# Performance work log

Measured on AMD Instinct MI355X. Metric: run time of the kernel, lower is better.

## Reference

```python
import jax, jax.numpy as jnp
import numpy as np

N = 100000  # nodes
EPS_BN = 1e-5
EPS_NORM = 1e-12


def sage_conv(x, edge_index, wl, bl, wr):
    # PyG SAGEConv (aggr='mean', normalize=True, project=False):
    # out = lin_l(mean_{j in N(i)} x_j) + lin_r(x_i); then L2-normalize rows.
    src, dst = edge_index[0], edge_index[1]
    msgs = x[src]                                            # [E, C] gather
    agg = jax.ops.segment_sum(msgs, dst, num_segments=N)     # [N, C]
    cnt = jax.ops.segment_sum(jnp.ones((edge_index.shape[1],), x.dtype), dst,
                              num_segments=N)                # [N]
    agg = agg / jnp.maximum(cnt, 1.0)[:, None]               # mean (0 for isolated)
    out = agg @ wl.T + bl + x @ wr.T                         # lin_l has bias, lin_r doesn't
    nrm = jnp.sqrt(jnp.sum(out * out, axis=-1, keepdims=True))
    return out / jnp.maximum(nrm, EPS_NORM)


def batch_norm(x, gamma, beta):
    # BatchNorm1d in training mode: batch stats, biased variance
    mean = jnp.mean(x, axis=0)
    var = jnp.mean((x - mean) ** 2, axis=0)
    return gamma * (x - mean) * jax.lax.rsqrt(var + EPS_BN) + beta


def setup_inputs() -> dict:
    key = jax.random.key(0)
    ks = jax.random.split(key, 9)
    C_in, C_h, C_out = 128, 128, 47
    E = 800000
    x = jax.random.normal(ks[0], (N, C_in), dtype=jnp.float32)
    edge_index = jax.random.randint(ks[1], (2, E), 0, N, dtype=jnp.int64)
    s = 0.1
    return {
        "x": x,
        "edge_index": edge_index,
        "w1l": jax.random.normal(ks[2], (C_h, C_in), dtype=jnp.float32) * s,
        "b1l": jnp.zeros((C_h,), dtype=jnp.float32),
        "w1r": jax.random.normal(ks[3], (C_h, C_in), dtype=jnp.float32) * s,
        "bn_gamma": jnp.ones((C_h,), dtype=jnp.float32),
        "bn_beta": jnp.zeros((C_h,), dtype=jnp.float32),
        "w2l": jax.random.normal(ks[4], (C_out, C_h), dtype=jnp.float32) * s,
        "b2l": jnp.zeros((C_out,), dtype=jnp.float32),
        "w2r": jax.random.normal(ks[5], (C_out, C_h), dtype=jnp.float32) * s,
    }


def reference(x, edge_index, w1l, b1l, w1r, bn_gamma, bn_beta, w2l, b2l, w2r):
    h = sage_conv(x, edge_index, w1l, b1l, w1r)   # [N, 128]
    h = batch_norm(h, bn_gamma, bn_beta)
    h = jax.nn.relu(h)
    # dropout p=0.0 -> identity
    out = sage_conv(h, edge_index, w2l, b2l, w2r)  # [N, 47]
    return out
```

## Files before the change

### kernel.cpp

```cpp
#include <hip/hip_runtime.h>
#include <cstdint>


typedef __attribute__((ext_vector_type(8))) short s8v;
typedef __attribute__((ext_vector_type(4))) short s4v;
typedef __attribute__((ext_vector_type(4))) float fx4;

#define CSR_CHUNK 8192
#define CSR_SH 8
#define CSR_NBPAD 512
#define CSR_BUFCAP 3072

static __device__ __forceinline__ float bf2f(unsigned short h) {
    union { unsigned int u; float f; } c; c.u = (unsigned int)h << 16; return c.f;
}
static __device__ __forceinline__ unsigned short f2bf(float f) {
    union { float f; unsigned int u; } c; c.f = f;
    unsigned int u = c.u;
    return (unsigned short)((u + 0x7FFF + ((u >> 16) & 1)) >> 16);
}

__global__ __launch_bounds__(256) void k_prep(
        const float* __restrict__ x, const float* __restrict__ w1l,
        const float* __restrict__ w1r, const float* __restrict__ w2l,
        const float* __restrict__ w2r, const int* __restrict__ ei,
        unsigned short* __restrict__ xb, unsigned short* __restrict__ wB1,
        unsigned short* __restrict__ wB2p, float* __restrict__ stats,
        int* __restrict__ counts, int n, int nE, int prepBlocks) {
    __shared__ int hist[CSR_NBPAD];
    int t = threadIdx.x;
    if ((int)blockIdx.x >= prepBlocks) {
        int chunk = blockIdx.x - prepBlocks;
        hist[t] = 0; hist[t + 256] = 0;
        __syncthreads();
        int e0 = chunk * CSR_CHUNK;
        int e1 = min(e0 + CSR_CHUNK, nE);
        for (int e = e0 + t; e < e1; e += 256)
            atomicAdd(&hist[ei[nE + e] >> CSR_SH], 1);
        __syncthreads();
        counts[chunk * CSR_NBPAD + t] = hist[t];
        counts[chunk * CSR_NBPAD + t + 256] = hist[t + 256];
        return;
    }
    int idx = blockIdx.x * 256 + t;
    int nx = n * 16;
    if (idx < nx) {
        float4 a = ((const float4*)x)[idx * 2];
        float4 b = ((const float4*)x)[idx * 2 + 1];
        union { s8v v; unsigned short u[8]; } o;
        o.u[0] = f2bf(a.x); o.u[1] = f2bf(a.y); o.u[2] = f2bf(a.z); o.u[3] = f2bf(a.w);
        o.u[4] = f2bf(b.x); o.u[5] = f2bf(b.y); o.u[6] = f2bf(b.z); o.u[7] = f2bf(b.w);
        ((s8v*)xb)[idx] = o.v;
        return;
    }
    idx -= nx;
    if (idx < 32768) {
        int j = idx >> 8, k = idx & 255;
        float v = (k < 128) ? w1l[j * 128 + k] : w1r[j * 128 + (k - 128)];
        wB1[idx] = f2bf(v);
        return;
    }
    idx -= 32768;
    if (idx < 16384) {
        int j = idx >> 7, k = idx & 127;
        float v = 0.f;
        if (j < 47)      v = w2l[j * 128 + k];
        else if (j < 94) v = w2r[(j - 47) * 128 + k];
        wB2p[idx] = f2bf(v);
        return;
    }
    idx -= 16384;
    if (idx < 256) stats[idx] = 0.f;
}

__global__ __launch_bounds__(256) void k_bmeta(
        const int* __restrict__ counts, int* __restrict__ bucketStart,
        int* __restrict__ gcur, int nCh, int NB) {
    __shared__ int tot[CSR_NBPAD], tot2[CSR_NBPAD], sh[256], bs[CSR_NBPAD];
    int t = threadIdx.x;
    int tl = t & 127, g = t >> 7;
    int half = (nCh + 1) >> 1;
    int c0 = g * half, c1 = min(nCh, c0 + half);
    int4 s4 = {0, 0, 0, 0};
    for (int c = c0; c < c1; ++c) {
        int4 v = *(const int4*)(counts + (size_t)c * CSR_NBPAD + tl * 4);
        s4.x += v.x; s4.y += v.y; s4.z += v.z; s4.w += v.w;
    }
    *(int4*)((g ? tot2 : tot) + tl * 4) = s4;
    __syncthreads();
    tot[t] += tot2[t];
    tot[t + 256] += tot2[t + 256];
    __syncthreads();
    int pairSum = tot[2 * t] + tot[2 * t + 1];
    sh[t] = pairSum;
    __syncthreads();
    for (int off = 1; off < 256; off <<= 1) {
        int add = (t >= off) ? sh[t - off] : 0;
        __syncthreads();
        sh[t] += add;
        __syncthreads();
    }
    int excl = sh[t] - pairSum;
    bs[2 * t] = excl;
    bs[2 * t + 1] = excl + tot[2 * t];
    __syncthreads();
    for (int b = t; b <= NB; b += 256) bucketStart[b] = bs[b];
    for (int b = t; b < CSR_NBPAD; b += 256) gcur[b] = bs[b];
}

__global__ __launch_bounds__(256) void k_bfill(
        const int* __restrict__ ei, const int* __restrict__ counts,
        int* __restrict__ gcur, int* __restrict__ pairs, int nE) {
    __shared__ int cur[CSR_NBPAD];
    int t = threadIdx.x;
    #pragma unroll
    for (int i = 0; i < 2; ++i) {
        int b = t + i * 256;
        int h = counts[blockIdx.x * CSR_NBPAD + b];
        cur[b] = h ? atomicAdd(&gcur[b], h) : 0;
    }
    __syncthreads();
    int e0 = blockIdx.x * CSR_CHUNK;
    int e1 = min(e0 + CSR_CHUNK, nE);
    for (int e = e0 + t; e < e1; e += 256) {
        int s = ei[e];
        int d = ei[nE + e];
        int p = atomicAdd(&cur[d >> CSR_SH], 1);
        pairs[p] = (s << 8) | (d & 255);
    }
}

__global__ __launch_bounds__(256) void k_csr(
        const int* __restrict__ pairs, const int* __restrict__ bucketStart,
        int* __restrict__ deg, int* __restrict__ rowStart,
        int* __restrict__ srcIdx, int n) {
    __shared__ int cnt[256], scn[256], cur[256];
    __shared__ int buf[CSR_BUFCAP];
    int t = threadIdx.x;
    int bkt = blockIdx.x;
    int eBeg = bucketStart[bkt], eEnd = bucketStart[bkt + 1];
    int node0 = bkt << CSR_SH;
    cnt[t] = 0;
    __syncthreads();
    for (int e = eBeg + t; e < eEnd; e += 256)
        atomicAdd(&cnt[pairs[e] & 255], 1);
    __syncthreads();
    int myc = cnt[t];
    scn[t] = myc;
    __syncthreads();
    for (int off = 1; off < 256; off <<= 1) {
        int add = (t >= off) ? scn[t - off] : 0;
        __syncthreads();
        scn[t] += add;
        __syncthreads();
    }
    int excl = scn[t] - myc;
    cur[t] = excl;
    int node = node0 + t;
    if (node < n) { deg[node] = myc; rowStart[node] = eBeg + excl; }
    __syncthreads();
    for (int e = eBeg + t; e < eEnd; e += 256) {
        int pk = pairs[e];
        int p = atomicAdd(&cur[pk & 255], 1);
        int src = pk >> 8;
        if (p < CSR_BUFCAP) buf[p] = src;
        else srcIdx[eBeg + p] = src;
    }
    __syncthreads();
    int m = min(eEnd - eBeg, CSR_BUFCAP);
    for (int i = t; i < m; i += 256) srcIdx[eBeg + i] = buf[i];
}

__global__ __launch_bounds__(256) void k_gather1(
        const unsigned short* __restrict__ xb, const int* __restrict__ rowStart,
        const int* __restrict__ deg, const int* __restrict__ srcIdx,
        unsigned short* __restrict__ aggb, int n) {
    int t = threadIdx.x;
    int q = t & 15, grp = t >> 4;
    int node = blockIdx.x * 16 + grp;
    if (node >= n) return;
    int beg = rowStart[node];
    int d = deg[node];
    int end = beg + d;
    float a0[8] = {}, a1[8] = {}, a2[8] = {}, a3[8] = {};
    int e = beg;
    for (; e + 4 <= end; e += 4) {
        int s0 = srcIdx[e], s1v = srcIdx[e + 1], s2 = srcIdx[e + 2], s3 = srcIdx[e + 3];
        s8v v0 = *(const s8v*)(xb + (size_t)s0 * 128 + q * 8);
        s8v v1 = *(const s8v*)(xb + (size_t)s1v * 128 + q * 8);
        s8v v2 = *(const s8v*)(xb + (size_t)s2 * 128 + q * 8);
        s8v v3 = *(const s8v*)(xb + (size_t)s3 * 128 + q * 8);
        #pragma unroll
        for (int u = 0; u < 8; ++u) {
            a0[u] += bf2f((unsigned short)v0[u]);
            a1[u] += bf2f((unsigned short)v1[u]);
            a2[u] += bf2f((unsigned short)v2[u]);
            a3[u] += bf2f((unsigned short)v3[u]);
        }
    }
    for (; e < end; ++e) {
        s8v v0 = *(const s8v*)(xb + (size_t)srcIdx[e] * 128 + q * 8);
        #pragma unroll
        for (int u = 0; u < 8; ++u) a0[u] += bf2f((unsigned short)v0[u]);
    }
    float ic = 1.0f / fmaxf((float)d, 1.0f);
    union { s8v v; unsigned short u[8]; } o;
    #pragma unroll
    for (int u = 0; u < 8; ++u)
        o.u[u] = f2bf((a0[u] + a1[u] + a2[u] + a3[u]) * ic);
    *(s8v*)(aggb + (size_t)node * 128 + q * 8) = o.v;
}

__global__ __launch_bounds__(256, 3) void k_gemm1(
        const unsigned short* __restrict__ xb, const unsigned short* __restrict__ aggb,
        const unsigned short* __restrict__ wB1, const float* __restrict__ b1l,
        unsigned short* __restrict__ s1b, float* __restrict__ stats, int n) {
    __shared__ float norm2[256];
    __shared__ float invn[128];
    __shared__ float statS[256];
    __shared__ float statQ[256];
    int t = threadIdx.x;
    int w = t >> 6, L = t & 63;
    int q = L >> 4, lm = L & 15;
    int wr0 = (w >> 1) * 64;
    int wc0 = (w & 1) * 64;
    int r0 = blockIdx.x * 128;

    int arow[4], brow[4];
    #pragma unroll
    for (int r = 0; r < 4; ++r) {
        int gr = r0 + wr0 + r * 16 + lm;
        arow[r] = gr < n ? gr : (n - 1);
        brow[r] = wc0 + r * 16 + lm;
    }

    fx4 acc[4][4];
    fx4 z4 = {0.f, 0.f, 0.f, 0.f};
    #pragma unroll
    for (int r = 0; r < 4; ++r)
        #pragma unroll
        for (int c = 0; c < 4; ++c) acc[r][c] = z4;

    #pragma unroll
    for (int kt = 0; kt < 8; ++kt) {
        const unsigned short* src = (kt < 4) ? aggb : xb;
        int kb = (kt & 3) * 32 + q * 8;
        s8v af[4], bfr[4];
        #pragma unroll
        for (int r = 0; r < 4; ++r)
            af[r] = *(const s8v*)(src + (size_t)arow[r] * 128 + kb);
        #pragma unroll
        for (int c = 0; c < 4; ++c)
            bfr[c] = *(const s8v*)(wB1 + (size_t)brow[c] * 256 + kt * 32 + q * 8);
        #pragma unroll
        for (int r = 0; r < 4; ++r)
            #pragma unroll
            for (int c = 0; c < 4; ++c)
                acc[r][c] = __builtin_amdgcn_mfma_f32_16x16x32_bf16(af[r], bfr[c], acc[r][c], 0, 0, 0);
    }

    float bj[4];
    #pragma unroll
    for (int c = 0; c < 4; ++c) bj[c] = b1l[wc0 + c * 16 + lm];
    #pragma unroll
    for (int r = 0; r < 4; ++r)
        #pragma unroll
        for (int c = 0; c < 4; ++c) acc[r][c] += bj[c];

    fx4 pr[4];
    #pragma unroll
    for (int r = 0; r < 4; ++r) {
        fx4 p = acc[r][0] * acc[r][0];
        #pragma unroll
        for (int c = 1; c < 4; ++c) p += acc[r][c] * acc[r][c];
        #pragma unroll
        for (int off = 1; off <= 8; off <<= 1)
            #pragma unroll
            for (int i2 = 0; i2 < 4; ++i2) p[i2] += __shfl_xor(p[i2], off, 64);
        pr[r] = p;
    }

    if (lm == 0) {
        #pragma unroll
        for (int r = 0; r < 4; ++r)
            #pragma unroll
            for (int i = 0; i < 4; ++i)
                norm2[(wr0 + r * 16 + q * 4 + i) * 2 + (w & 1)] = pr[r][i];
    }
    __syncthreads();
    if (t < 128) {
        float s = norm2[t * 2] + norm2[t * 2 + 1];
        invn[t] = 1.0f / fmaxf(sqrtf(s), 1e-12f);
    }
    __syncthreads();

    float cS[4] = {}, cQ[4] = {};
    #pragma unroll
    for (int r = 0; r < 4; ++r) {
        int rowb = wr0 + r * 16 + q * 4;
        fx4 iv = *(const fx4*)&invn[rowb];
        #pragma unroll
        for (int c = 0; c < 4; ++c) {
            fx4 v = acc[r][c] * iv;
            int col = wc0 + c * 16 + lm;
            #pragma unroll
            for (int i = 0; i < 4; ++i) {
                int gr = r0 + rowb + i;
                if (gr < n) {
                    s1b[(size_t)gr * 128 + col] = f2bf(v[i]);
                    cS[c] += v[i];
                    cQ[c] += v[i] * v[i];
                }
            }
        }
    }
    #pragma unroll
    for (int off = 16; off <= 32; off <<= 1)
        #pragma unroll
        for (int c = 0; c < 4; ++c) {
            cS[c] += __shfl_xor(cS[c], off, 64);
            cQ[c] += __shfl_xor(cQ[c], off, 64);
        }
    if (q == 0) {
        #pragma unroll
        for (int c = 0; c < 4; ++c) {
            int col = wc0 + c * 16 + lm;
            statS[col * 2 + (w >> 1)] = cS[c];
            statQ[col * 2 + (w >> 1)] = cQ[c];
        }
    }
    __syncthreads();
    if (t < 128) {
        atomicAdd(&stats[t],       statS[t * 2] + statS[t * 2 + 1]);
        atomicAdd(&stats[128 + t], statQ[t * 2] + statQ[t * 2 + 1]);
    }
}

__global__ __launch_bounds__(256, 3) void k_gemm2(
        const unsigned short* __restrict__ s1b, const unsigned short* __restrict__ wB2p,
        const float* __restrict__ stats, const float* __restrict__ gamma,
        const float* __restrict__ beta, const float* __restrict__ b2l,
        unsigned short* __restrict__ y2b, float* __restrict__ rbuf, int n) {
    __shared__ __align__(16) float abuf[128];
    __shared__ __align__(16) float bbuf[128];
    int t = threadIdx.x;
    int w = t >> 6, L = t & 63;
    int q = L >> 4, lm = L & 15;
    int wr0 = (w >> 1) * 64, wc0 = (w & 1) * 64;
    int r0 = blockIdx.x * 128;

    if (t < 128) {
        float s = stats[t], qv = stats[128 + t];
        float fn = (float)n;
        float mean = s / fn;
        float var = qv / fn - mean * mean;
        float istd = rsqrtf(var + 1e-5f);
        float a = gamma[t] * istd;
        abuf[t] = a;
        bbuf[t] = beta[t] - mean * a;
    }
    __syncthreads();

    int arow[4], brow[4];
    #pragma unroll
    for (int r = 0; r < 4; ++r) {
        int gr = r0 + wr0 + r * 16 + lm;
        arow[r] = gr < n ? gr : (n - 1);
        brow[r] = wc0 + r * 16 + lm;
    }

    fx4 acc[4][4];
    fx4 z4 = {0.f, 0.f, 0.f, 0.f};
    #pragma unroll
    for (int r = 0; r < 4; ++r)
        #pragma unroll
        for (int c = 0; c < 4; ++c) acc[r][c] = z4;

    #pragma unroll
    for (int kt = 0; kt < 4; ++kt) {
        int kb = kt * 32 + q * 8;
        fx4 a0 = *(const fx4*)&abuf[kb];
        fx4 a1 = *(const fx4*)&abuf[kb + 4];
        fx4 b0 = *(const fx4*)&bbuf[kb];
        fx4 b1 = *(const fx4*)&bbuf[kb + 4];
        s8v af[4], bfr[4];
        #pragma unroll
        for (int r = 0; r < 4; ++r) {
            s8v sv = *(const s8v*)(s1b + (size_t)arow[r] * 128 + kb);
            union { s8v v; unsigned short u[8]; } o;
            #pragma unroll
            for (int u = 0; u < 4; ++u) {
                float h0 = fmaxf(fmaf(a0[u], bf2f((unsigned short)sv[u]), b0[u]), 0.f);
                float h1 = fmaxf(fmaf(a1[u], bf2f((unsigned short)sv[u + 4]), b1[u]), 0.f);
                o.u[u]     = f2bf(h0);
                o.u[u + 4] = f2bf(h1);
            }
            af[r] = o.v;
        }
        #pragma unroll
        for (int c = 0; c < 4; ++c)
            bfr[c] = *(const s8v*)(wB2p + (size_t)brow[c] * 128 + kb);
        #pragma unroll
        for (int r = 0; r < 4; ++r)
            #pragma unroll
            for (int c = 0; c < 4; ++c)
                acc[r][c] = __builtin_amdgcn_mfma_f32_16x16x32_bf16(af[r], bfr[c], acc[r][c], 0, 0, 0);
    }

    #pragma unroll
    for (int c = 0; c < 4; ++c) {
        int col = wc0 + c * 16 + lm;
        float bb = (col >= 47 && col < 94) ? b2l[col - 47] : 0.f;
        #pragma unroll
        for (int r = 0; r < 4; ++r) {
            int rowb = wr0 + r * 16 + q * 4;
            #pragma unroll
            for (int i = 0; i < 4; ++i) {
                int gr = r0 + rowb + i;
                if (gr >= n) continue;
                float v = acc[r][c][i];
                if (col < 47)      y2b[(size_t)gr * 64 + col] = f2bf(v);
                else if (col < 94) rbuf[(size_t)gr * 48 + (col - 47)] = v + bb;
            }
        }
    }
}

__global__ __launch_bounds__(256) void k_gather2_final(
        const unsigned short* __restrict__ y2b, const float* __restrict__ rbuf,
        const int* __restrict__ rowStart, const int* __restrict__ deg,
        const int* __restrict__ srcIdx, float* __restrict__ out, int n) {
    int t = threadIdx.x;
    int q = t & 15, grp = t >> 4;
    int node = blockIdx.x * 16 + grp;
    if (node >= n) return;
    int beg = rowStart[node];
    int d = deg[node];
    int end = beg + d;
    float acc[4] = {0.f, 0.f, 0.f, 0.f};
    int e = beg;
    for (; e + 8 <= end; e += 8) {
        int s0 = srcIdx[e],     s1v = srcIdx[e + 1];
        int s2 = srcIdx[e + 2], s3  = srcIdx[e + 3];
        int s4 = srcIdx[e + 4], s5  = srcIdx[e + 5];
        int s6 = srcIdx[e + 6], s7  = srcIdx[e + 7];
        s4v v0 = *(const s4v*)(y2b + (size_t)s0 * 64 + q * 4);
        s4v v1 = *(const s4v*)(y2b + (size_t)s1v * 64 + q * 4);
        s4v v2 = *(const s4v*)(y2b + (size_t)s2 * 64 + q * 4);
        s4v v3 = *(const s4v*)(y2b + (size_t)s3 * 64 + q * 4);
        s4v v4 = *(const s4v*)(y2b + (size_t)s4 * 64 + q * 4);
        s4v v5 = *(const s4v*)(y2b + (size_t)s5 * 64 + q * 4);
        s4v v6 = *(const s4v*)(y2b + (size_t)s6 * 64 + q * 4);
        s4v v7 = *(const s4v*)(y2b + (size_t)s7 * 64 + q * 4);
        #pragma unroll
        for (int u = 0; u < 4; ++u) {
            acc[u] += (bf2f((unsigned short)v0[u]) + bf2f((unsigned short)v1[u]))
                    + (bf2f((unsigned short)v2[u]) + bf2f((unsigned short)v3[u]))
                    + (bf2f((unsigned short)v4[u]) + bf2f((unsigned short)v5[u]))
                    + (bf2f((unsigned short)v6[u]) + bf2f((unsigned short)v7[u]));
        }
    }
    for (; e + 4 <= end; e += 4) {
        int s0 = srcIdx[e],     s1v = srcIdx[e + 1];
        int s2 = srcIdx[e + 2], s3  = srcIdx[e + 3];
        s4v v0 = *(const s4v*)(y2b + (size_t)s0 * 64 + q * 4);
        s4v v1 = *(const s4v*)(y2b + (size_t)s1v * 64 + q * 4);
        s4v v2 = *(const s4v*)(y2b + (size_t)s2 * 64 + q * 4);
        s4v v3 = *(const s4v*)(y2b + (size_t)s3 * 64 + q * 4);
        #pragma unroll
        for (int u = 0; u < 4; ++u)
            acc[u] += (bf2f((unsigned short)v0[u]) + bf2f((unsigned short)v1[u]))
                    + (bf2f((unsigned short)v2[u]) + bf2f((unsigned short)v3[u]));
    }
    for (; e < end; ++e) {
        s4v v0 = *(const s4v*)(y2b + (size_t)srcIdx[e] * 64 + q * 4);
        #pragma unroll
        for (int u = 0; u < 4; ++u) acc[u] += bf2f((unsigned short)v0[u]);
    }
    float ic = 1.0f / fmaxf((float)d, 1.0f);
    fx4 rb = *(const fx4*)(rbuf + (size_t)node * 48 + q * 4);
    float vi[4];
    float ss = 0.f;
    #pragma unroll
    for (int u = 0; u < 4; ++u) {
        int ch = q * 4 + u;
        float v = (ch < 47) ? (acc[u] * ic + rb[u]) : 0.f;
        vi[u] = v;
        ss += v * v;
    }
    #pragma unroll
    for (int off = 1; off <= 8; off <<= 1) ss += __shfl_xor(ss, off, 64);
    float inv = 1.0f / fmaxf(sqrtf(ss), 1e-12f);
    #pragma unroll
    for (int u = 0; u < 4; ++u) {
        int ch = q * 4 + u;
        if (ch < 47) out[(size_t)node * 47 + ch] = vi[u] * inv;
    }
}

extern "C" void kernel_launch(void* const* d_in, const int* in_sizes, int n_in,
                              void* d_out, int out_size, void* d_ws, size_t ws_size,
                              hipStream_t stream) {
    const float* x     = (const float*)d_in[0];
    const int*   ei    = (const int*)d_in[1];
    const float* w1l   = (const float*)d_in[2];
    const float* b1l   = (const float*)d_in[3];
    const float* w1r   = (const float*)d_in[4];
    const float* gamma = (const float*)d_in[5];
    const float* beta  = (const float*)d_in[6];
    const float* w2l   = (const float*)d_in[7];
    const float* b2l   = (const float*)d_in[8];
    const float* w2r   = (const float*)d_in[9];
    float* out = (float*)d_out;

    int n  = in_sizes[0] / 128;
    int nE = in_sizes[1] / 2;

    int NB  = (n + 255) >> 8;
    int nCh = (nE + CSR_CHUNK - 1) / CSR_CHUNK;

    int* deg       = (int*)d_ws;
    float* stats   = (float*)(deg + n);
    int* rowStart  = (int*)(stats + 256);
    int* meta      = rowStart + n;
    int* srcIdx    = meta + n;
    unsigned short* xb   = (unsigned short*)(srcIdx + nE);
    unsigned short* aggb = xb + (size_t)n * 128;
    unsigned short* s1b  = aggb + (size_t)n * 128;
    unsigned short* wB1  = s1b + (size_t)n * 128;
    unsigned short* wB2p = wB1 + 32768;
    int* counts      = meta;
    int* bucketStart = meta + 60000;
    int* gcur        = meta + 61000;
    int* pairs       = (int*)s1b;
    unsigned short* y2b = xb;
    float* rbuf = (float*)(y2b + (size_t)n * 64);

    int prepTotal  = n * 16 + 32768 + 16384 + 256;
    int prepBlocks = (prepTotal + 255) / 256;

    k_prep<<<prepBlocks + nCh, 256, 0, stream>>>(
        x, w1l, w1r, w2l, w2r, ei, xb, wB1, wB2p, stats, counts, n, nE, prepBlocks);
    k_bmeta<<<1, 256, 0, stream>>>(counts, bucketStart, gcur, nCh, NB);
    k_bfill<<<nCh, 256, 0, stream>>>(ei, counts, gcur, pairs, nE);
    k_csr<<<NB, 256, 0, stream>>>(pairs, bucketStart, deg, rowStart, srcIdx, n);
    k_gather1<<<(n + 15) / 16, 256, 0, stream>>>(xb, rowStart, deg, srcIdx, aggb, n);
    k_gemm1<<<(n + 127) / 128, 256, 0, stream>>>(xb, aggb, wB1, b1l, s1b, stats, n);
    k_gemm2<<<(n + 127) / 128, 256, 0, stream>>>(
        s1b, wB2p, stats, gamma, beta, b2l, y2b, rbuf, n);
    k_gather2_final<<<(n + 15) / 16, 256, 0, stream>>>(y2b, rbuf, rowStart, deg, srcIdx, out, n);
}
```

Measured before the change: 298.7 us.

## Stage GEMM operand tiles in LDS via async global_load_lds with XOR swizzle

Both GEMM kernels now copy their whole A tile (aggregated/input features or layer-1 activations) and the weight tile into shared memory with direct global-to-LDS 16-byte loads before computing. Previously each lane read its MFMA fragments straight from global memory. The layout uses an XOR swizzle to avoid bank conflicts, and the loads are issued up front so they can coalesce. In exchange, LDS use rises sharply (about 128 KB in gemm1), occupancy bounds drop to 1 and 2 blocks per CU, and there is no overlap between the copy and the compute.

```diff
diff --git a/kernel.cpp b/kernel.cpp
--- a/kernel.cpp
+++ b/kernel.cpp
@@ -211,10 +211,17 @@
     *(s8v*)(aggb + (size_t)node * 128 + q * 8) = o.v;
 }
 
-__global__ __launch_bounds__(256, 3) void k_gemm1(
+#define GLL16(GSRC, LDST) \
+    __builtin_amdgcn_global_load_lds( \
+        (__attribute__((address_space(1))) void*)(void*)(GSRC), \
+        (__attribute__((address_space(3))) void*)(LDST), 16, 0, 0)
+
+__global__ __launch_bounds__(256, 1) void k_gemm1(
         const unsigned short* __restrict__ xb, const unsigned short* __restrict__ aggb,
         const unsigned short* __restrict__ wB1, const float* __restrict__ b1l,
         unsigned short* __restrict__ s1b, float* __restrict__ stats, int n) {
+    __shared__ __align__(16) unsigned short xs[128 * 256];
+    __shared__ __align__(16) unsigned short ws[128 * 256];
     __shared__ float norm2[256];
     __shared__ float invn[128];
     __shared__ float statS[256];
@@ -226,13 +233,16 @@
     int wc0 = (w & 1) * 64;
     int r0 = blockIdx.x * 128;
 
-    int arow[4], brow[4];
-    #pragma unroll
-    for (int r = 0; r < 4; ++r) {
-        int gr = r0 + wr0 + r * 16 + lm;
-        arow[r] = gr < n ? gr : (n - 1);
-        brow[r] = wc0 + r * 16 + lm;
-    }
+    for (int i = t; i < 4096; i += 256) {
+        int row = i >> 5, p = i & 31;
+        int sl = p ^ (row & 7);
+        int gr = r0 + row; gr = gr < n ? gr : (n - 1);
+        const unsigned short* sp = (sl < 16) ? (aggb + (size_t)gr * 128 + sl * 8)
+                                             : (xb + (size_t)gr * 128 + (sl - 16) * 8);
+        GLL16(sp, &xs[i * 8]);
+        GLL16(wB1 + (size_t)row * 256 + sl * 8, &ws[i * 8]);
+    }
+    __syncthreads();
 
     fx4 acc[4][4];
     fx4 z4 = {0.f, 0.f, 0.f, 0.f};
@@ -243,15 +253,18 @@
 
     #pragma unroll
     for (int kt = 0; kt < 8; ++kt) {
-        const unsigned short* src = (kt < 4) ? aggb : xb;
-        int kb = (kt & 3) * 32 + q * 8;
+        int slot = kt * 4 + q;
         s8v af[4], bfr[4];
         #pragma unroll
-        for (int r = 0; r < 4; ++r)
-            af[r] = *(const s8v*)(src + (size_t)arow[r] * 128 + kb);
-        #pragma unroll
-        for (int c = 0; c < 4; ++c)
-            bfr[c] = *(const s8v*)(wB1 + (size_t)brow[c] * 256 + kt * 32 + q * 8);
+        for (int r = 0; r < 4; ++r) {
+            int row = wr0 + r * 16 + lm;
+            af[r] = *(const s8v*)&xs[row * 256 + ((slot ^ (row & 7)) << 3)];
+        }
+        #pragma unroll
+        for (int c = 0; c < 4; ++c) {
+            int row = wc0 + c * 16 + lm;
+            bfr[c] = *(const s8v*)&ws[row * 256 + ((slot ^ (row & 7)) << 3)];
+        }
         #pragma unroll
         for (int r = 0; r < 4; ++r)
             #pragma unroll
@@ -336,11 +349,13 @@
     }
 }
 
-__global__ __launch_bounds__(256, 3) void k_gemm2(
+__global__ __launch_bounds__(256, 2) void k_gemm2(
         const unsigned short* __restrict__ s1b, const unsigned short* __restrict__ wB2p,
         const float* __restrict__ stats, const float* __restrict__ gamma,
         const float* __restrict__ beta, const float* __restrict__ b2l,
         unsigned short* __restrict__ y2b, float* __restrict__ rbuf, int n) {
+    __shared__ __align__(16) unsigned short xs[128 * 128];
+    __shared__ __align__(16) unsigned short ws[128 * 128];
     __shared__ __align__(16) float abuf[128];
     __shared__ __align__(16) float bbuf[128];
     int t = threadIdx.x;
@@ -359,15 +374,15 @@
         abuf[t] = a;
         bbuf[t] = beta[t] - mean * a;
     }
-    __syncthreads();
-
-    int arow[4], brow[4];
-    #pragma unroll
-    for (int r = 0; r < 4; ++r) {
-        int gr = r0 + wr0 + r * 16 + lm;
-        arow[r] = gr < n ? gr : (n - 1);
-        brow[r] = wc0 + r * 16 + lm;
-    }
+
+    for (int i = t; i < 2048; i += 256) {
+        int row = i >> 4, p = i & 15;
+        int sl = p ^ (row & 7);
+        int gr = r0 + row; gr = gr < n ? gr : (n - 1);
+        GLL16(s1b + (size_t)gr * 128 + sl * 8, &xs[i * 8]);
+        GLL16(wB2p + (size_t)row * 128 + sl * 8, &ws[i * 8]);
+    }
+    __syncthreads();
 
     fx4 acc[4][4];
     fx4 z4 = {0.f, 0.f, 0.f, 0.f};
@@ -378,6 +393,7 @@
 
     #pragma unroll
     for (int kt = 0; kt < 4; ++kt) {
+        int slot = kt * 4 + q;
         int kb = kt * 32 + q * 8;
         fx4 a0 = *(const fx4*)&abuf[kb];
         fx4 a1 = *(const fx4*)&abuf[kb + 4];
@@ -386,7 +402,8 @@
         s8v af[4], bfr[4];
         #pragma unroll
         for (int r = 0; r < 4; ++r) {
-            s8v sv = *(const s8v*)(s1b + (size_t)arow[r] * 128 + kb);
+            int row = wr0 + r * 16 + lm;
+            s8v sv = *(const s8v*)&xs[row * 128 + ((slot ^ (row & 7)) << 3)];
             union { s8v v; unsigned short u[8]; } o;
             #pragma unroll
             for (int u = 0; u < 4; ++u) {
@@ -398,8 +415,10 @@
             af[r] = o.v;
         }
         #pragma unroll
-        for (int c = 0; c < 4; ++c)
-            bfr[c] = *(const s8v*)(wB2p + (size_t)brow[c] * 128 + kb);
+        for (int c = 0; c < 4; ++c) {
+            int row = wc0 + c * 16 + lm;
+            bfr[c] = *(const s8v*)&ws[row * 128 + ((slot ^ (row & 7)) << 3)];
+        }
         #pragma unroll
         for (int r = 0; r < 4; ++r)
             #pragma unroll
```

Result: faster. 291.8 us (-2.3%).
